# Performance work log

Measured on AMD Instinct MI355X. Metric: run time of the kernel, lower is better.

Reference implementation:

```python
import jax, jax.numpy as jnp
import numpy as np
from jax import lax

O, C, K = 256, 64, 3          # out_channels, in_channels, kernel size
M = 9                          # ALSH augmentation terms (m)
EXTRA = M // (K * K)           # channels Q appends to the input (=1)
D = C + EXTRA                  # d = in_channels + m/(k*k)
T = 8192                       # table_size
R = 4.0                        # hash bucket width hash.r
STRIDE, PAD = 1, 1


def _P(kernels):
    # ALSH preprocessing: flatten each kernel and append powers of its squared norm
    flat = kernels.reshape(O, -1)                        # [O, C*K*K]
    n2 = jnp.sum(flat * flat, axis=1, keepdims=True)     # [O, 1]
    pows = jnp.concatenate([n2 ** (i + 1) for i in range(M)], axis=1)  # [O, M]
    return jnp.concatenate([flat, pows], axis=1)         # [O, C*K*K + M]


def _hash(a, b, x):
    # x: [n, C*K*K + M];  floor((a . x + b) / r)
    return jnp.floor((x @ a + b) / R)


def setup_inputs():
    key = jax.random.key(0)
    k1, k2, k3, k4 = jax.random.split(key, 4)
    inp = jax.random.normal(k1, (16, C, 256, 256), jnp.float32)
    kernels = jax.random.normal(k2, (O, C, K, K), jnp.float32) * 0.04
    a = jax.random.normal(k3, (D * K * K,), jnp.float32)
    b = jax.random.uniform(k4, (1,), jnp.float32) * R
    return {"input": inp, "kernels": kernels, "a": a, "b": b}


def reference(input, kernels, a, b):
    N, _, H, W = input.shape
    # ---- init_table: hash every kernel into a bucket (vectorized scatter) ----
    hk = _hash(a, b[0], _P(kernels))                     # [O]
    idx = jnp.abs(jnp.fmod(hk, T)).astype(jnp.int32)     # torch: fmod_ then abs_
    onehot = jax.nn.one_hot(idx, T, dtype=jnp.int32)     # [O, T]
    excl = jnp.cumsum(onehot, axis=0) - onehot           # slot within bucket (insertion order)
    pos = jnp.take_along_axis(excl, idx[:, None], axis=1)[:, 0]
    table = jnp.zeros((T, 2 * O), jnp.int32).at[idx, pos].set(
        jnp.arange(O, dtype=jnp.int32))
    row_len = jnp.sum(onehot, axis=0)                    # [T] bucket sizes
    # ---- vote: hash every conv patch via a 1-output-channel convolution ----
    inp_q = jnp.concatenate(
        [input, jnp.full((N, EXTRA, H, W), 0.5, input.dtype)], axis=1)  # Q(input)
    kern = a.reshape(1, D, K, K)
    dotted = lax.conv_general_dilated(inp_q, kern, (STRIDE, STRIDE),
                                      [(PAD, PAD), (PAD, PAD)])
    votes = jnp.floor((dotted.reshape(-1) + b[0]) / R)   # [N*H'*W']
    vidx = jnp.abs(jnp.fmod(votes, T)).astype(jnp.int32)
    count = jax.ops.segment_sum(jnp.ones_like(votes), vidx, num_segments=T)
    index = jnp.argmax(count)
    # ---- gather active set (fixed-size padded gather, sorted rows) ----
    L = row_len[index]
    slot = jnp.arange(2 * O)
    rows = jnp.where(slot < L, table[index], O)          # sentinel O sorts to the end
    rows = jnp.sort(rows)
    valid = (slot < L).astype(kernels.dtype)
    active = kernels[jnp.clip(rows, 0, O - 1)] * valid[:, None, None, None]
    return active, count, index.astype(jnp.int32)
```

## Files before the change

kernel.cpp:

```cpp
#include <hip/hip_runtime.h>

#define O_CH   256
#define C_CH   64
#define FLATK  576
#define M_TERMS 9
#define AL     585
#define TSZ    8192
#define RADIUS 4.0f
#define NB     16
#define HH     256
#define WW     256

#define WS_KIDX 0
#define WS_HIST 256
#define WS_BEST (256 + TSZ)
#define WS_ROWS (256 + TSZ + 2)

__global__ __launch_bounds__(256) void k_init(const float* __restrict__ kernels,
                                              const float* __restrict__ a,
                                              const float* __restrict__ b,
                                              int* __restrict__ ws) {
    if (blockIdx.x < 64) {
        const int wv = threadIdx.x >> 6, lane = threadIdx.x & 63;
        const int o = blockIdx.x * 4 + wv;
        const float* wp = kernels + o * FLATK;
        float dot = 0.f, n2 = 0.f;
        #pragma unroll
        for (int j0 = 0; j0 < FLATK; j0 += 64) {
            float x = wp[j0 + lane];
            dot += x * a[j0 + lane];
            n2  += x * x;
        }
        #pragma unroll
        for (int off = 32; off > 0; off >>= 1) {
            dot += __shfl_xor(dot, off);
            n2  += __shfl_xor(n2, off);
        }
        if (lane == 0) {
            float p = n2, d = dot;
            for (int i = 0; i < M_TERMS; ++i) { d += p * a[FLATK + i]; p *= n2; }
            float hk = floorf((d + b[0]) / RADIUS);
            ws[WS_KIDX + o] = (int)fabsf(fmodf(hk, (float)TSZ));
        }
    } else {
        int t = (blockIdx.x - 64) * 256 + threadIdx.x;
        ws[WS_HIST + t] = 0;
        if (blockIdx.x == 64 && threadIdx.x < 2) ws[WS_BEST + threadIdx.x] = 0;
    }
}

#define TILE_H 8
__global__ __launch_bounds__(512, 4) void k_vote(const float* __restrict__ input,
                                                 const float* __restrict__ a,
                                                 const float* __restrict__ b,
                                                 int* __restrict__ ws) {
    __shared__ int   hist_s[TSZ];
    __shared__ float a_s[AL];
    const int tid = threadIdx.x;

    for (int i = tid; i < TSZ; i += 512) hist_s[i] = 0;
    for (int i = tid; i < AL; i += 512) a_s[i] = a[i];
    __syncthreads();

    const float bv = b[0];
    const int t   = (blockIdx.x & 7) * 64 + (blockIdx.x >> 3);
    const int by  = t & 31;
    const int n   = t >> 5;
    const int y0  = by * TILE_H;
    const int lane = tid & 63;
    const int wv  = tid >> 6;
    const int x4  = lane * 4;
    const int y   = y0 + wv;

    float acc[4] = {0.f, 0.f, 0.f, 0.f};
    const float* imgbase = input + (size_t)n * C_CH * HH * WW;

    float4 vbuf[2][3];
    {
        const float* src = imgbase;
        #pragma unroll
        for (int r = 0; r < 3; ++r) {
            int gy = y - 1 + r;
            vbuf[0][r] = (gy >= 0 && gy < HH)
                       ? *(const float4*)(src + gy * WW + x4)
                       : make_float4(0.f, 0.f, 0.f, 0.f);
        }
    }

    #pragma unroll 2
    for (int c = 0; c < C_CH; ++c) {
        const int cur = c & 1, nxt = cur ^ 1;
        if (c + 1 < C_CH) {
            const float* src = imgbase + (size_t)(c + 1) * (HH * WW);
            #pragma unroll
            for (int r = 0; r < 3; ++r) {
                int gy = y - 1 + r;
                vbuf[nxt][r] = (gy >= 0 && gy < HH)
                             ? *(const float4*)(src + gy * WW + x4)
                             : make_float4(0.f, 0.f, 0.f, 0.f);
            }
        }
        const float* ac = a_s + c * 9;
        #pragma unroll
        for (int r = 0; r < 3; ++r) {
            float4 v = vbuf[cur][r];
            float lv = __shfl_up(v.w, 1);   if (lane == 0)  lv = 0.f;
            float rv = __shfl_down(v.x, 1); if (lane == 63) rv = 0.f;
            const float w[6] = {lv, v.x, v.y, v.z, v.w, rv};
            #pragma unroll
            for (int p = 0; p < 4; ++p)
                #pragma unroll
                for (int kx = 0; kx < 3; ++kx)
                    acc[p] += w[p + kx] * ac[r * 3 + kx];
        }
    }

    {
        int gy = y;
        #pragma unroll
        for (int p = 0; p < 4; ++p) {
            int gx = x4 + p;
            float cs = 0.f;
            #pragma unroll
            for (int ky = 0; ky < 3; ++ky) {
                int yy = gy + ky - 1;
                if (yy < 0 || yy >= HH) continue;
                #pragma unroll
                for (int kx = 0; kx < 3; ++kx) {
                    int xx = gx + kx - 1;
                    if (xx < 0 || xx >= WW) continue;
                    cs += a_s[FLATK + ky * 3 + kx];
                }
            }
            float tt = acc[p] + 0.5f * cs;
            float v = floorf((tt + bv) / RADIUS);
            int vi = (int)fabsf(fmodf(v, (float)TSZ));
            atomicAdd(&hist_s[vi], 1);
        }
    }

    __syncthreads();
    int* hist_g = ws + WS_HIST;
    for (int i = tid; i < TSZ; i += 512) {
        int v = hist_s[i];
        if (v) atomicAdd(&hist_g[i], v);
    }
}

__global__ __launch_bounds__(256) void k_argmax(const int* __restrict__ ws,
                                                int* __restrict__ wsbest,
                                                float* __restrict__ out) {
    const int tid = threadIdx.x;
    const int t = blockIdx.x * 256 + tid;
    const int v = ws[WS_HIST + t];
    out[512 * FLATK + t] = (float)v;

    unsigned long long key =
        ((unsigned long long)(unsigned)v << 13) | (unsigned)(TSZ - 1 - t);
    #pragma unroll
    for (int off = 32; off > 0; off >>= 1) {
        unsigned long long o = __shfl_xor(key, off);
        if (o > key) key = o;
    }
    __shared__ unsigned long long wk[4];
    const int lane = tid & 63, wvi = tid >> 6;
    if (lane == 0) wk[wvi] = key;
    __syncthreads();
    if (tid == 0) {
        unsigned long long k = wk[0];
        for (int i = 1; i < 4; ++i) if (wk[i] > k) k = wk[i];
        atomicMax((unsigned long long*)(wsbest + WS_BEST), k);
    }
}

__global__ __launch_bounds__(256) void k_rows(int* __restrict__ ws,
                                              float* __restrict__ out) {
    __shared__ int wsum[4];
    const int tid = threadIdx.x;
    const unsigned long long key = *(const unsigned long long*)(ws + WS_BEST);
    const int bestIdx = (TSZ - 1) - (int)(key & (unsigned long long)(TSZ - 1));
    if (tid == 0) out[512 * FLATK + TSZ] = (float)bestIdx;

    int* rows = ws + WS_ROWS;
    for (int i = tid; i < 2 * O_CH; i += 256) rows[i] = -1;
    const int o = tid;
    const int match = (ws[WS_KIDX + o] == bestIdx) ? 1 : 0;
    unsigned long long m = __ballot(match);
    const int lane = tid & 63, wvi = tid >> 6;
    if (lane == 0) wsum[wvi] = __popcll(m);
    __syncthreads();
    int prefix = 0;
    for (int i = 0; i < wvi; ++i) prefix += wsum[i];
    int before = __popcll(m & ((1ull << lane) - 1ull));
    if (match) rows[prefix + before] = o;
}

__global__ __launch_bounds__(256) void k_gather(const float* __restrict__ kernels,
                                                const int* __restrict__ ws,
                                                float* __restrict__ out) {
    int gid = blockIdx.x * 256 + threadIdx.x;
    if (gid >= 2 * O_CH * (FLATK / 4)) return;
    int s = gid / (FLATK / 4);
    int j = gid - s * (FLATK / 4);
    int r = ws[WS_ROWS + s];
    float4 v = (r >= 0) ? *(const float4*)(kernels + r * FLATK + j * 4)
                        : make_float4(0.f, 0.f, 0.f, 0.f);
    *((float4*)out + gid) = v;
}

extern "C" void kernel_launch(void* const* d_in, const int* in_sizes, int n_in,
                              void* d_out, int out_size, void* d_ws, size_t ws_size,
                              hipStream_t stream) {
    const float* input   = (const float*)d_in[0];
    const float* kernels = (const float*)d_in[1];
    const float* a       = (const float*)d_in[2];
    const float* b       = (const float*)d_in[3];
    float* out = (float*)d_out;
    int*   ws  = (int*)d_ws;

    k_init<<<96, 256, 0, stream>>>(kernels, a, b, ws);
    k_vote<<<NB * (HH / TILE_H), 512, 0, stream>>>(input, a, b, ws);
    k_argmax<<<TSZ / 256, 256, 0, stream>>>(ws, ws, out);
    k_rows<<<1, 256, 0, stream>>>(ws, out);
    k_gather<<<(2 * O_CH * (FLATK / 4) + 255) / 256, 256, 0, stream>>>(kernels, ws, out);
}
```

Measured before the change: 380.2 us.

## Shrink vote histogram LDS, split columns across blocks, fuse row selection into gather

The vote kernel's shared histogram shrinks from 8192 to 1024 bins, and out-of-range bins go straight to global atomics. The point is to cut LDS per block, raise occupancy, and shorten the zero and flush loops. Each block now covers half a row width with float2 loads and explicit halo loads, so the grid doubles. A 3-stage register load/compute rotation over channels replaces the 2-deep buffer. The separate k_rows kernel is folded into k_gather, which saves a launch at the cost of every block recomputing the ballot over kernel indices. Votes landing in high bins now pay for slower global atomics.

```diff
diff --git a/kernel.cpp b/kernel.cpp
--- a/kernel.cpp
+++ b/kernel.cpp
@@ -6,6 +6,7 @@
 #define M_TERMS 9
 #define AL     585
 #define TSZ    8192
+#define HSZ    1024
 #define RADIUS 4.0f
 #define NB     16
 #define HH     256
@@ -14,7 +15,6 @@
 #define WS_KIDX 0
 #define WS_HIST 256
 #define WS_BEST (256 + TSZ)
-#define WS_ROWS (256 + TSZ + 2)
 
 __global__ __launch_bounds__(256) void k_init(const float* __restrict__ kernels,
                                               const float* __restrict__ a,
@@ -54,94 +54,105 @@
                                                  const float* __restrict__ a,
                                                  const float* __restrict__ b,
                                                  int* __restrict__ ws) {
-    __shared__ int   hist_s[TSZ];
+    __shared__ int   hist_s[HSZ];
     __shared__ float a_s[AL];
     const int tid = threadIdx.x;
 
-    for (int i = tid; i < TSZ; i += 512) hist_s[i] = 0;
+    for (int i = tid; i < HSZ; i += 512) hist_s[i] = 0;
     for (int i = tid; i < AL; i += 512) a_s[i] = a[i];
     __syncthreads();
 
     const float bv = b[0];
-    const int t   = (blockIdx.x & 7) * 64 + (blockIdx.x >> 3);
-    const int by  = t & 31;
-    const int n   = t >> 5;
-    const int y0  = by * TILE_H;
+    int* hist_g = ws + WS_HIST;
+    const int t    = (blockIdx.x & 7) * 128 + (blockIdx.x >> 3);
+    const int xs   = t & 1;
+    const int by   = (t >> 1) & 31;
+    const int n    = t >> 6;
     const int lane = tid & 63;
-    const int wv  = tid >> 6;
-    const int x4  = lane * 4;
-    const int y   = y0 + wv;
-
-    float acc[4] = {0.f, 0.f, 0.f, 0.f};
+    const int wv   = tid >> 6;
+    const int y    = by * TILE_H + wv;
+    const int x2   = xs * 128 + lane * 2;
+
+    const bool isE = (lane == 0) | (lane == 63);
+    const int  hx  = (lane == 0) ? (x2 - 1) : (x2 + 2);
+    const bool hok = isE && ((lane == 0) ? (x2 > 0) : (x2 + 2 < WW));
+
+    float acc[2] = {0.f, 0.f};
     const float* imgbase = input + (size_t)n * C_CH * HH * WW;
 
-    float4 vbuf[2][3];
-    {
-        const float* src = imgbase;
+    float2 v0[3], v1[3], v2[3];
+    float  h0[3], h1[3], h2[3];
+
+#define LOADCH(c, VB, HB)                                                     \
+    if ((c) < C_CH) {                                                         \
+        const float* src = imgbase + (size_t)(c) * (HH * WW);                 \
+        _Pragma("unroll")                                                     \
+        for (int r = 0; r < 3; ++r) {                                         \
+            int gy = y - 1 + r;                                               \
+            bool ok = (gy >= 0 && gy < HH);                                   \
+            const float* rp = src + gy * WW;                                  \
+            VB[r] = ok ? *(const float2*)(rp + x2) : make_float2(0.f, 0.f);   \
+            HB[r] = (ok && hok) ? rp[hx] : 0.f;                               \
+        }                                                                     \
+    }
+
+#define COMPCH(c, VB, HB)                                                     \
+    {                                                                         \
+        const float* ac = a_s + (c) * 9;                                      \
+        _Pragma("unroll")                                                     \
+        for (int r = 0; r < 3; ++r) {                                         \
+            float2 v = VB[r];                                                 \
+            float lv = __shfl_up(v.y, 1);                                     \
+            float rv = __shfl_down(v.x, 1);                                   \
+            if (lane == 0)  lv = HB[r];                                       \
+            if (lane == 63) rv = HB[r];                                       \
+            acc[0] += lv  * ac[r * 3 + 0];                                    \
+            acc[0] += v.x * ac[r * 3 + 1];                                    \
+            acc[0] += v.y * ac[r * 3 + 2];                                    \
+            acc[1] += v.x * ac[r * 3 + 0];                                    \
+            acc[1] += v.y * ac[r * 3 + 1];                                    \
+            acc[1] += rv  * ac[r * 3 + 2];                                    \
+        }                                                                     \
+    }
+
+    LOADCH(0, v0, h0)
+    LOADCH(1, v1, h1)
+    for (int c3 = 0; c3 < 63; c3 += 3) {
+        LOADCH(c3 + 2, v2, h2)
+        COMPCH(c3 + 0, v0, h0)
+        LOADCH(c3 + 3, v0, h0)
+        COMPCH(c3 + 1, v1, h1)
+        LOADCH(c3 + 4, v1, h1)
+        COMPCH(c3 + 2, v2, h2)
+    }
+    COMPCH(63, v0, h0)
+#undef LOADCH
+#undef COMPCH
+
+    #pragma unroll
+    for (int p = 0; p < 2; ++p) {
+        int gx = x2 + p;
+        float cs = 0.f;
         #pragma unroll
-        for (int r = 0; r < 3; ++r) {
-            int gy = y - 1 + r;
-            vbuf[0][r] = (gy >= 0 && gy < HH)
-                       ? *(const float4*)(src + gy * WW + x4)
-                       : make_float4(0.f, 0.f, 0.f, 0.f);
-        }
-    }
-
-    #pragma unroll 2
-    for (int c = 0; c < C_CH; ++c) {
-        const int cur = c & 1, nxt = cur ^ 1;
-        if (c + 1 < C_CH) {
-            const float* src = imgbase + (size_t)(c + 1) * (HH * WW);
+        for (int ky = 0; ky < 3; ++ky) {
+            int yy = y + ky - 1;
+            if (yy < 0 || yy >= HH) continue;
             #pragma unroll
-            for (int r = 0; r < 3; ++r) {
-                int gy = y - 1 + r;
-                vbuf[nxt][r] = (gy >= 0 && gy < HH)
-                             ? *(const float4*)(src + gy * WW + x4)
-                             : make_float4(0.f, 0.f, 0.f, 0.f);
+            for (int kx = 0; kx < 3; ++kx) {
+                int xx = gx + kx - 1;
+                if (xx < 0 || xx >= WW) continue;
+                cs += a_s[FLATK + ky * 3 + kx];
             }
         }
-        const float* ac = a_s + c * 9;
-        #pragma unroll
-        for (int r = 0; r < 3; ++r) {
-            float4 v = vbuf[cur][r];
-            float lv = __shfl_up(v.w, 1);   if (lane == 0)  lv = 0.f;
-            float rv = __shfl_down(v.x, 1); if (lane == 63) rv = 0.f;
-            const float w[6] = {lv, v.x, v.y, v.z, v.w, rv};
-            #pragma unroll
-            for (int p = 0; p < 4; ++p)
-                #pragma unroll
-                for (int kx = 0; kx < 3; ++kx)
-                    acc[p] += w[p + kx] * ac[r * 3 + kx];
-        }
-    }
-
-    {
-        int gy = y;
-        #pragma unroll
-        for (int p = 0; p < 4; ++p) {
-            int gx = x4 + p;
-            float cs = 0.f;
-            #pragma unroll
-            for (int ky = 0; ky < 3; ++ky) {
-                int yy = gy + ky - 1;
-                if (yy < 0 || yy >= HH) continue;
-                #pragma unroll
-                for (int kx = 0; kx < 3; ++kx) {
-                    int xx = gx + kx - 1;
-                    if (xx < 0 || xx >= WW) continue;
-                    cs += a_s[FLATK + ky * 3 + kx];
-                }
-            }
-            float tt = acc[p] + 0.5f * cs;
-            float v = floorf((tt + bv) / RADIUS);
-            int vi = (int)fabsf(fmodf(v, (float)TSZ));
-            atomicAdd(&hist_s[vi], 1);
-        }
-    }
-
-    __syncthreads();
-    int* hist_g = ws + WS_HIST;
-    for (int i = tid; i < TSZ; i += 512) {
+        float tt = acc[p] + 0.5f * cs;
+        float v = floorf((tt + bv) / RADIUS);
+        int vi = (int)fabsf(fmodf(v, (float)TSZ));
+        if (vi < HSZ) atomicAdd(&hist_s[vi], 1);
+        else          atomicAdd(&hist_g[vi], 1);
+    }
+
+    __syncthreads();
+    for (int i = tid; i < HSZ; i += 512) {
         int v = hist_s[i];
         if (v) atomicAdd(&hist_g[i], v);
     }
@@ -173,18 +184,18 @@
     }
 }
 
-__global__ __launch_bounds__(256) void k_rows(int* __restrict__ ws,
-                                              float* __restrict__ out) {
+__global__ __launch_bounds__(256) void k_gather(const float* __restrict__ kernels,
+                                                const int* __restrict__ ws,
+                                                float* __restrict__ out) {
+    __shared__ int rows_s[2 * O_CH];
     __shared__ int wsum[4];
     const int tid = threadIdx.x;
     const unsigned long long key = *(const unsigned long long*)(ws + WS_BEST);
     const int bestIdx = (TSZ - 1) - (int)(key & (unsigned long long)(TSZ - 1));
-    if (tid == 0) out[512 * FLATK + TSZ] = (float)bestIdx;
-
-    int* rows = ws + WS_ROWS;
-    for (int i = tid; i < 2 * O_CH; i += 256) rows[i] = -1;
-    const int o = tid;
-    const int match = (ws[WS_KIDX + o] == bestIdx) ? 1 : 0;
+    if (blockIdx.x == 0 && tid == 0) out[512 * FLATK + TSZ] = (float)bestIdx;
+
+    for (int i = tid; i < 2 * O_CH; i += 256) rows_s[i] = -1;
+    const int match = (ws[WS_KIDX + tid] == bestIdx) ? 1 : 0;
     unsigned long long m = __ballot(match);
     const int lane = tid & 63, wvi = tid >> 6;
     if (lane == 0) wsum[wvi] = __popcll(m);
@@ -192,20 +203,18 @@
     int prefix = 0;
     for (int i = 0; i < wvi; ++i) prefix += wsum[i];
     int before = __popcll(m & ((1ull << lane) - 1ull));
-    if (match) rows[prefix + before] = o;
-}
-
-__global__ __launch_bounds__(256) void k_gather(const float* __restrict__ kernels,
-                                                const int* __restrict__ ws,
-                                                float* __restrict__ out) {
-    int gid = blockIdx.x * 256 + threadIdx.x;
-    if (gid >= 2 * O_CH * (FLATK / 4)) return;
-    int s = gid / (FLATK / 4);
-    int j = gid - s * (FLATK / 4);
-    int r = ws[WS_ROWS + s];
-    float4 v = (r >= 0) ? *(const float4*)(kernels + r * FLATK + j * 4)
-                        : make_float4(0.f, 0.f, 0.f, 0.f);
-    *((float4*)out + gid) = v;
+    if (match) rows_s[prefix + before] = tid;
+    __syncthreads();
+
+    int gid = blockIdx.x * 256 + tid;
+    if (gid < 2 * O_CH * (FLATK / 4)) {
+        int s = gid / (FLATK / 4);
+        int j = gid - s * (FLATK / 4);
+        int r = rows_s[s];
+        float4 v = (r >= 0) ? *(const float4*)(kernels + r * FLATK + j * 4)
+                            : make_float4(0.f, 0.f, 0.f, 0.f);
+        *((float4*)out + gid) = v;
+    }
 }
 
 extern "C" void kernel_launch(void* const* d_in, const int* in_sizes, int n_in,
@@ -219,8 +228,7 @@
     int*   ws  = (int*)d_ws;
 
     k_init<<<96, 256, 0, stream>>>(kernels, a, b, ws);
-    k_vote<<<NB * (HH / TILE_H), 512, 0, stream>>>(input, a, b, ws);
+    k_vote<<<NB * (HH / TILE_H) * 2, 512, 0, stream>>>(input, a, b, ws);
     k_argmax<<<TSZ / 256, 256, 0, stream>>>(ws, ws, out);
-    k_rows<<<1, 256, 0, stream>>>(ws, out);
     k_gather<<<(2 * O_CH * (FLATK / 4) + 255) / 256, 256, 0, stream>>>(kernels, ws, out);
 }
```

Result: slower. 396.7 us (+4.3%).
